# Kernel optimization log

Measured on AMD Instinct MI355X. Metric: run time of the kernel, lower is better.

The kernel has to match this reference:

```python
import jax, jax.numpy as jnp
import numpy as np

B, L, DIM, HEADS = 4, 1024, 512, 8
HD = DIM // HEADS
HID = max(64, DIM // 2)
WIN = 32
SPARSITY = 0.3
TEMP = 1.0
PAT_TAU = 0.5


def setup_inputs() -> dict:
    key = jax.random.key(0)
    ks = jax.random.split(key, 8)
    gn = lambda k, shape, sc: jax.random.normal(k, shape, jnp.float32) * sc
    return {
        "x": jax.random.normal(ks[0], (B, L, DIM), jnp.float32),
        "mask": jnp.ones((B, L), jnp.int32),
        "Wqkv": gn(ks[1], (3 * DIM, DIM), 0.02),
        "Wproj": gn(ks[2], (DIM, DIM), 0.02),
        "bproj": jnp.zeros((DIM,), jnp.float32),
        "Wsel1": gn(ks[3], (HID, DIM), 0.05),
        "bsel1": jnp.zeros((HID,), jnp.float32),
        "Wsel2": gn(ks[4], (3, HID), 0.05),
        "bsel2": jnp.zeros((3,), jnp.float32),
        "log_pattern_tau": jnp.asarray(np.log(PAT_TAU), jnp.float32),
        "sparse_w": gn(ks[5], (HEADS,), 0.2),
        "sparse_b": jnp.zeros((HEADS,), jnp.float32),
    }


def reference(x, mask, Wqkv, Wproj, bproj, Wsel1, bsel1, Wsel2, bsel2,
              log_pattern_tau, sparse_w, sparse_b):
    Bq, Lq, D = x.shape
    scale = HD ** -0.5
    qkv = (x @ Wqkv.T).reshape(Bq, Lq, 3, HEADS, HD)
    q = jnp.transpose(qkv[:, :, 0], (0, 2, 1, 3))  # (B,H,L,hd)
    k = jnp.transpose(qkv[:, :, 1], (0, 2, 1, 3))
    v = jnp.transpose(qkv[:, :, 2], (0, 2, 1, 3))
    scores = jnp.einsum('bhid,bhjd->bhij', q, k) * scale  # (B,H,L,L)

    # pattern selector on mean-pooled features (eval: no gumbel, no dropout)
    pooled = x.mean(axis=1)
    logits = jax.nn.relu(pooled @ Wsel1.T + bsel1) @ Wsel2.T + bsel2  # (B,3)
    tau = jnp.clip(jnp.exp(log_pattern_tau), 1e-4, 10.0)
    pw = jax.nn.softmax(logits / tau, axis=-1)  # (B,3)

    half = WIN // 2
    ii = jnp.arange(Lq)[:, None]
    jj = jnp.arange(Lq)[None, :]
    local = ((jj >= ii - half) & (jj <= ii + half)).astype(jnp.float32)

    # learned sparse top-k mask per head via kth-value threshold
    kk = max(1, int(Lq * (1.0 - SPARSITY)))
    s = scores * sparse_w[None, :, None, None] + sparse_b[None, :, None, None]
    kth = jax.lax.top_k(s, kk)[0][..., -1:]
    smask = (s >= kth).astype(jnp.float32)  # (B,H,L,L)

    combined = (pw[:, 0, None, None, None] * local[None, None]
                + pw[:, 1, None, None, None]
                + pw[:, 2, None, None, None] * smask)
    neg = jnp.float32(-1e9)
    scores = jnp.where(combined > 0.05, scores, neg)
    scores = jnp.where(mask[:, None, None, :] == 0, neg, scores)

    # fallback: if a row is fully masked, unmask position 0
    all_masked = jnp.all(scores <= neg + 1e-6, axis=-1)  # (B,H,L)
    scores = scores.at[..., 0].set(jnp.where(all_masked, 0.0, scores[..., 0]))

    attn = jax.nn.softmax(scores / TEMP, axis=-1)
    out = jnp.einsum('bhij,bhjd->bhid', attn, v)
    out = jnp.transpose(out, (0, 2, 1, 3)).reshape(Bq, Lq, D)
    return out @ Wproj.T + bproj
```

## Files before the change

kernel.cpp:

```cpp
#include <hip/hip_runtime.h>
#include <math.h>

typedef __attribute__((ext_vector_type(8))) short short8;
typedef __attribute__((ext_vector_type(4))) float floatx4;

#define MFMA16(a, b, c) __builtin_amdgcn_mfma_f32_16x16x32_bf16(a, b, c, 0, 0, 0)


#define FRAG512(row, k) (((size_t)((row) >> 4)) * 8192 + (((k) >> 5) * 512) + \
                         ((((k) >> 3) & 3) * 128) + (((row) & 15) * 8) + ((k) & 7))
#define FRAGQK(row, e)  (((size_t)((row) >> 4)) * 1024 + (((e) >> 5) * 512) + \
                         ((((e) >> 3) & 3) * 128) + (((row) & 15) * 8) + ((e) & 7))

#define OFF_XB    ((size_t)0)
#define OFF_WQKV  ((size_t)4194304)
#define OFF_WPROJ ((size_t)5767168)
#define OFF_Q     ((size_t)6291456)
#define OFF_K     ((size_t)10485760)
#define OFF_VT    ((size_t)14680064)
#define OFF_AT    ((size_t)18874368)
#define OFF_PW    ((size_t)23068672)
#define OFF_PAR   ((size_t)23069696)
#define OFF_W1T   ((size_t)23595008)

__device__ __forceinline__ unsigned short f2bf(float f) {
    unsigned u = __float_as_uint(f);
    return (unsigned short)((u + 0x7fffu + ((u >> 16) & 1u)) >> 16);
}
__device__ __forceinline__ float bf2f(unsigned short s) {
    return __uint_as_float((unsigned)s << 16);
}
__device__ __forceinline__ void gl16(const void* g, void* l) {
    __builtin_amdgcn_global_load_lds(
        (const __attribute__((address_space(1))) unsigned*)g,
        (__attribute__((address_space(3))) unsigned*)l, 16, 0, 0);
}

__device__ __forceinline__ void frag_cvt_tile(const float* __restrict__ src,
                                              unsigned short* __restrict__ dst,
                                              const int t, const float sc)
{
    const int ln = t & 15, quad = (t >> 4) & 3, kh = t >> 6;
    #pragma unroll
    for (int i = 0; i < 4; ++i) {
        const int kb = kh + i * 4;
        const float* s = src + (size_t)ln * 512 + kb * 32 + quad * 8;
        float4 f0 = *(const float4*)s;
        float4 f1 = *(const float4*)(s + 4);
        unsigned short o[8] = { f2bf(f0.x * sc), f2bf(f0.y * sc), f2bf(f0.z * sc), f2bf(f0.w * sc),
                                f2bf(f1.x * sc), f2bf(f1.y * sc), f2bf(f1.z * sc), f2bf(f1.w * sc) };
        unsigned short* d = dst + kb * 512 + (size_t)(t & 63) * 8;
        *(ushort4*)d       = make_ushort4(o[0], o[1], o[2], o[3]);
        *(ushort4*)(d + 4) = make_ushort4(o[4], o[5], o[6], o[7]);
    }
}

__global__ __launch_bounds__(256)
void cvt_all(const float* __restrict__ x, const float* __restrict__ wqkv,
             const float* __restrict__ wproj, const float* __restrict__ W1,
             unsigned short* __restrict__ xb, unsigned short* __restrict__ oq,
             unsigned short* __restrict__ op, float* __restrict__ partial,
             float* __restrict__ w1t)
{
    const int bid = blockIdx.x, t = threadIdx.x;
    if (bid < 256) {
        const int rt = bid;
        const float* src = x + (size_t)rt * 16 * 512;
        frag_cvt_tile(src, xb + (size_t)rt * 8192, t, 1.f);
        float s0 = 0.f, s1 = 0.f;
        #pragma unroll 4
        for (int l = 0; l < 16; ++l) {
            s0 += src[(size_t)l * 512 + t];
            s1 += src[(size_t)l * 512 + t + 256];
        }
        partial[(size_t)rt * 512 + t] = s0;
        partial[(size_t)rt * 512 + t + 256] = s1;
    } else if (bid < 384) {
        const int tile = bid - 256;
        if (tile < 96)
            frag_cvt_tile(wqkv + (size_t)tile * 16 * 512, oq + (size_t)tile * 8192, t, 1.f);
        else
            frag_cvt_tile(wproj + (size_t)(tile - 96) * 16 * 512,
                          op + (size_t)(tile - 96) * 8192, t, 1.f);
    } else {
        __shared__ float tl[64][65];
        const int tile = bid - 384;
        const int tr = tile >> 3, tc = tile & 7;
        const int lr = t >> 6, lc = t & 63;
        #pragma unroll
        for (int p = 0; p < 16; ++p) {
            const int r = p * 4 + lr;
            tl[r][lc] = W1[(size_t)(tr * 64 + r) * 512 + tc * 64 + lc];
        }
        __syncthreads();
        #pragma unroll
        for (int p = 0; p < 16; ++p) {
            const int d = p * 4 + lr;
            w1t[(size_t)(tc * 64 + d) * 256 + tr * 64 + lc] = tl[lc][d];
        }
    }
}

__global__ __launch_bounds__(128)
void gemm_qkv_sel(const unsigned short* __restrict__ xb, const unsigned short* __restrict__ wb,
                  unsigned short* __restrict__ qo, unsigned short* __restrict__ ko,
                  unsigned short* __restrict__ vo,
                  const float* __restrict__ partial, const float* __restrict__ w1t,
                  const float* __restrict__ b1, const float* __restrict__ W2,
                  const float* __restrict__ b2, const float* __restrict__ ltau,
                  float* __restrict__ pwout)
{
    __shared__ __align__(16) unsigned short tile[2][64 * 72];
    const int bx = blockIdx.x, by = blockIdx.y;
    const int t = threadIdx.x;
    const int w = t >> 6, l64 = t & 63;

    if (by == 64) {
        if (bx >= 4) return;
        const int b = bx;
        float* pooled = (float*)&tile[0][0];
        float* hpart  = pooled + 512;
        float* h1s    = hpart + 512;
        float* lg     = h1s + 256;
        #pragma unroll
        for (int c = 0; c < 4; ++c) {
            const int col = t + c * 128;
            float s = 0.f;
            for (int p = 0; p < 64; ++p) s += partial[((size_t)b * 64 + p) * 512 + col];
            pooled[col] = s * (1.f / 1024.f);
        }
        __syncthreads();
        {
            float4 acc = make_float4(0.f, 0.f, 0.f, 0.f);
            const float* wt = w1t + (size_t)w * 256 * 256 + l64 * 4;
            for (int d = 0; d < 256; ++d) {
                const float pv = pooled[w * 256 + d];
                float4 wv = *(const float4*)(wt + (size_t)d * 256);
                acc.x += pv * wv.x; acc.y += pv * wv.y;
                acc.z += pv * wv.z; acc.w += pv * wv.w;
            }
            *(float4*)&hpart[w * 256 + l64 * 4] = acc;
        }
        __syncthreads();
        {
            #pragma unroll
            for (int c = 0; c < 2; ++c) {
                const int r = t + c * 128;
                h1s[r] = fmaxf(hpart[r] + hpart[256 + r] + b1[r], 0.f);
            }
        }
        __syncthreads();
        if (t < 3) {
            float s = b2[t];
            const float* w2 = W2 + t * 256;
            for (int i = 0; i < 256; ++i) s += w2[i] * h1s[i];
            float tauv = fminf(fmaxf(expf(ltau[0]), 1e-4f), 10.f);
            lg[t] = s / tauv;
        }
        __syncthreads();
        if (t == 0) {
            float m = fmaxf(lg[0], fmaxf(lg[1], lg[2]));
            float e0 = expf(lg[0] - m), e1 = expf(lg[1] - m), e2 = expf(lg[2] - m);
            float inv = 1.f / (e0 + e1 + e2);
            pwout[b * 3 + 0] = e0 * inv;
            pwout[b * 3 + 1] = e1 * inv;
            pwout[b * 3 + 2] = e2 * inv;
        }
        return;
    }

    const int ln = l64 & 15, quad = l64 >> 4;
    const int m0 = by << 6;
    const int nb0 = (bx << 7) + (w << 6);

    const unsigned short* Abase = xb + ((size_t)(m0 >> 4)) * 8192 + l64 * 8;
    const unsigned short* Bbase = wb + ((size_t)(nb0 >> 4)) * 8192 + l64 * 8;

    floatx4 acc[4][4];
    #pragma unroll
    for (int i = 0; i < 4; ++i)
        #pragma unroll
        for (int j = 0; j < 4; ++j) acc[i][j] = (floatx4){0.f, 0.f, 0.f, 0.f};

    short8 a0[4], b0[4], a1[4], b1v[4];
    #pragma unroll
    for (int i = 0; i < 4; ++i) {
        a0[i] = *(const short8*)(Abase + (size_t)i * 8192);
        b0[i] = *(const short8*)(Bbase + (size_t)i * 8192);
    }
    for (int s = 0; s < 16; s += 2) {
        #pragma unroll
        for (int i = 0; i < 4; ++i) {
            a1[i]  = *(const short8*)(Abase + (size_t)i * 8192 + (s + 1) * 512);
            b1v[i] = *(const short8*)(Bbase + (size_t)i * 8192 + (s + 1) * 512);
        }
        #pragma unroll
        for (int i = 0; i < 4; ++i)
            #pragma unroll
            for (int j = 0; j < 4; ++j)
                acc[i][j] = MFMA16(a0[i], b0[j], acc[i][j]);
        if (s + 2 < 16) {
            #pragma unroll
            for (int i = 0; i < 4; ++i) {
                a0[i] = *(const short8*)(Abase + (size_t)i * 8192 + (s + 2) * 512);
                b0[i] = *(const short8*)(Bbase + (size_t)i * 8192 + (s + 2) * 512);
            }
        }
        #pragma unroll
        for (int i = 0; i < 4; ++i)
            #pragma unroll
            for (int j = 0; j < 4; ++j)
                acc[i][j] = MFMA16(a1[i], b1v[j], acc[i][j]);
    }

    unsigned short* tw = &tile[w][0];
    const int which = bx >> 2;
    const int hh = (nb0 >> 6) & 7;
    const int g = (by >> 4) * 8 + hh;
    const int lrow0 = m0 & 1023;

    if (which == 2) {
        #pragma unroll
        for (int j = 0; j < 4; ++j)
            #pragma unroll
            for (int i = 0; i < 4; ++i)
                #pragma unroll
                for (int reg = 0; reg < 4; ++reg)
                    tw[(j * 16 + ln) * 72 + i * 16 + quad * 4 + reg] = f2bf(acc[i][j][reg]);
        const int chunk = lrow0 >> 7;
        const int ks0 = (lrow0 & 127) >> 5;
        unsigned short* dst = vo + (size_t)g * 65536 + (size_t)chunk * 8192;
        #pragma unroll
        for (int et = 0; et < 4; ++et)
            #pragma unroll
            for (int ksl = 0; ksl < 2; ++ksl) {
                const unsigned short* srcp = &tw[(et * 16 + ln) * 72 + ksl * 32 + quad * 8];
                *(short8*)(dst + (et * 4 + ks0 + ksl) * 512 + l64 * 8) = *(const short8*)srcp;
            }
    } else {
        const float sc = (which == 0) ? 0.125f : 1.f;
        #pragma unroll
        for (int j = 0; j < 4; ++j)
            #pragma unroll
            for (int i = 0; i < 4; ++i)
                #pragma unroll
                for (int reg = 0; reg < 4; ++reg)
                    tw[(i * 16 + quad * 4 + reg) * 72 + j * 16 + ln] = f2bf(acc[i][j][reg] * sc);
        unsigned short* dst = (which == 0 ? qo : ko) + (size_t)g * 65536;
        #pragma unroll
        for (int rt = 0; rt < 4; ++rt)
            #pragma unroll
            for (int eh = 0; eh < 2; ++eh) {
                const unsigned short* srcp = &tw[(rt * 16 + ln) * 72 + eh * 32 + quad * 8];
                *(short8*)(dst + ((size_t)((lrow0 >> 4) + rt)) * 1024 + eh * 512 + l64 * 8) =
                    *(const short8*)srcp;
            }
    }
}

__global__ __launch_bounds__(64)
void gemm_proj(const unsigned short* __restrict__ ab, const unsigned short* __restrict__ wb,
               const float* __restrict__ bias, float* __restrict__ out)
{
    const int t = threadIdx.x;
    const int ln = t & 15, quad = t >> 4;
    const int n0 = blockIdx.x << 6, m0 = blockIdx.y << 5;

    const unsigned short* Abase = ab + ((size_t)(m0 >> 4)) * 8192 + t * 8;
    const unsigned short* Bbase = wb + ((size_t)(n0 >> 4)) * 8192 + t * 8;

    floatx4 acc[2][4];
    #pragma unroll
    for (int i = 0; i < 2; ++i)
        #pragma unroll
        for (int j = 0; j < 4; ++j) acc[i][j] = (floatx4){0.f, 0.f, 0.f, 0.f};

    short8 a0[2], b0[4], a1[2], b1v[4];
    #pragma unroll
    for (int i = 0; i < 2; ++i) a0[i] = *(const short8*)(Abase + (size_t)i * 8192);
    #pragma unroll
    for (int j = 0; j < 4; ++j) b0[j] = *(const short8*)(Bbase + (size_t)j * 8192);
    for (int s = 0; s < 16; s += 2) {
        #pragma unroll
        for (int i = 0; i < 2; ++i) a1[i]  = *(const short8*)(Abase + (size_t)i * 8192 + (s + 1) * 512);
        #pragma unroll
        for (int j = 0; j < 4; ++j) b1v[j] = *(const short8*)(Bbase + (size_t)j * 8192 + (s + 1) * 512);
        #pragma unroll
        for (int i = 0; i < 2; ++i)
            #pragma unroll
            for (int j = 0; j < 4; ++j)
                acc[i][j] = MFMA16(a0[i], b0[j], acc[i][j]);
        if (s + 2 < 16) {
            #pragma unroll
            for (int i = 0; i < 2; ++i) a0[i] = *(const short8*)(Abase + (size_t)i * 8192 + (s + 2) * 512);
            #pragma unroll
            for (int j = 0; j < 4; ++j) b0[j] = *(const short8*)(Bbase + (size_t)j * 8192 + (s + 2) * 512);
        }
        #pragma unroll
        for (int i = 0; i < 2; ++i)
            #pragma unroll
            for (int j = 0; j < 4; ++j)
                acc[i][j] = MFMA16(a1[i], b1v[j], acc[i][j]);
    }
    #pragma unroll
    for (int j = 0; j < 4; ++j) {
        const float bv = bias[n0 + j * 16 + ln];
        #pragma unroll
        for (int i = 0; i < 2; ++i)
            #pragma unroll
            for (int reg = 0; reg < 4; ++reg)
                out[(size_t)(m0 + i * 16 + quad * 4 + reg) * 512 + n0 + j * 16 + ln] =
                    acc[i][j][reg] + bv;
    }
}

__global__ __launch_bounds__(256)
void attn_flash(const unsigned short* __restrict__ qm, const unsigned short* __restrict__ km,
                const unsigned short* __restrict__ vm, const int* __restrict__ mask,
                const float* __restrict__ pw, const float* __restrict__ sw,
                const float* __restrict__ sb, unsigned short* __restrict__ aout)
{
    __shared__ int mk[1024];
    __shared__ __align__(16) unsigned short Ks[8192];
    __shared__ __align__(16) unsigned short Vs[8192];
    __shared__ float PO[4][16][68];
    __shared__ unsigned kths[4][16];

    const int t = threadIdx.x;
    const int w = t >> 6, l64 = t & 63;
    const int ln = l64 & 15, quad = l64 >> 4;
    const int g = blockIdx.x & 31;
    const int rg = blockIdx.x >> 5;
    const int b = g >> 3, h = g & 7;
    const int i0 = rg * 64 + w * 16;

    const unsigned short* qg = qm + (size_t)g * 65536;
    const unsigned short* kg = km + (size_t)g * 65536;
    const unsigned short* vg = vm + (size_t)g * 65536;

    *(int4*)&mk[t * 4] = *(const int4*)(mask + b * 1024 + t * 4);

    const float pw0 = pw[b * 3 + 0], pw1 = pw[b * 3 + 1], pw2 = pw[b * 3 + 2];
    const bool a00 = pw1 > 0.05f;
    const bool a10 = (pw0 * 1.0f + pw1) > 0.05f;
    const bool a01 = (pw1 + pw2) > 0.05f;
    const bool a11 = ((pw0 * 1.0f + pw1) + pw2) > 0.05f;
    const bool need_sparse = (!a00 && a01) || (!a10 && a11);
    const bool flat_ok = (!need_sparse) && a00 && a10;
    const float w_h = sw[h], b_h = sb[h];
    __syncthreads();

    unsigned kth_r[4] = {0u, 0u, 0u, 0u};
    if (need_sparse) {
        unsigned* ub = (unsigned*)&PO[w][0][0];
        for (int r = 0; r < 16; ++r) {
            for (int c = 0; c < 16; ++c) {
                const int col = c * 64 + l64;
                float s = 0.f;
                for (int e = 0; e < 64; ++e)
                    s += bf2f(qg[FRAGQK(i0 + r, e)]) * bf2f(kg[FRAGQK(col, e)]);
                unsigned uu = __float_as_uint(s * w_h + b_h);
                ub[col] = (uu & 0x80000000u) ? ~uu : (uu | 0x80000000u);
            }
            unsigned u[16];
            #pragma unroll
            for (int c = 0; c < 16; ++c) u[c] = ub[l64 + c * 64];
            unsigned act = 0xFFFFu, p = 0u;
            int kk = 716;
            for (int bit = 31; bit >= 0; --bit) {
                unsigned ones = 0u;
                #pragma unroll
                for (int c = 0; c < 16; ++c)
                    if (((act >> c) & 1u) && ((u[c] >> bit) & 1u)) ones |= (1u << c);
                int c1 = __popc(ones);
                for (int off = 32; off; off >>= 1) c1 += __shfl_xor(c1, off);
                if (kk <= c1) { p |= (1u << bit); act &= ones; }
                else          { kk -= c1; act &= ~ones; }
            }
            if (l64 == 0) kths[w][r] = p;
        }
        #pragma unroll
        for (int reg = 0; reg < 4; ++reg) kth_r[reg] = kths[w][quad * 4 + reg];
    }

    const short8 aq0 = *(const short8*)(qg + ((size_t)(i0 >> 4)) * 1024 + l64 * 8);
    const short8 aq1 = *(const short8*)(qg + ((size_t)(i0 >> 4)) * 1024 + 512 + l64 * 8);

    float l_acc[4] = {0.f, 0.f, 0.f, 0.f};
    floatx4 accv[4];
    #pragma unroll
    for (int et = 0; et < 4; ++et) accv[et] = (floatx4){0.f, 0.f, 0.f, 0.f};
    unsigned short* Pw = (unsigned short*)&PO[w][0][0];

    for (int jc = 0; jc < 8; ++jc) {
        const int j0 = jc << 7;
        {
            const unsigned short* kc = kg + (size_t)j0 * 64;
            const unsigned short* vc = vg + ((size_t)(j0 >> 7)) * 8192;
            #pragma unroll
            for (int c = 0; c < 4; ++c) {
                const int bi = w * 4 + c;
                gl16(kc + bi * 512 + l64 * 8, (char*)Ks + bi * 1024);
                gl16(vc + bi * 512 + l64 * 8, (char*)Vs + bi * 1024);
            }
        }
        const bool mall = __all((mk[j0 + l64] != 0) && (mk[j0 + 64 + l64] != 0));
        const bool fast = flat_ok && mall;
        __syncthreads();

        floatx4 sfr[8];
        #pragma unroll
        for (int nt = 0; nt < 8; ++nt) {
            const short8 kb0 = *(const short8*)(Ks + nt * 1024 + l64 * 8);
            const short8 kb1 = *(const short8*)(Ks + nt * 1024 + 512 + l64 * 8);
            floatx4 z = (floatx4){0.f, 0.f, 0.f, 0.f};
            z = MFMA16(aq0, kb0, z);
            z = MFMA16(aq1, kb1, z);
            sfr[nt] = z;
        }

        if (!fast) {
            #pragma unroll
            for (int nt = 0; nt < 8; ++nt) {
                const int j = j0 + nt * 16 + ln;
                const bool mk0 = (mk[j] == 0);
                #pragma unroll
                for (int reg = 0; reg < 4; ++reg) {
                    const int i = i0 + quad * 4 + reg;
                    const float s = sfr[nt][reg];
                    const bool loc = (j >= i - 16) && (j <= i + 16);
                    bool sm = false;
                    if (need_sparse) {
                        unsigned uu = __float_as_uint(s * w_h + b_h);
                        unsigned key = (uu & 0x80000000u) ? ~uu : (uu | 0x80000000u);
                        sm = key >= kth_r[reg];
                    }
                    bool allowed = loc ? (sm ? a11 : a10) : (sm ? a01 : a00);
                    if (mk0) allowed = false;
                    sfr[nt][reg] = allowed ? s : -1e9f;
                }
            }
        }
        #pragma unroll
        for (int nt = 0; nt < 8; ++nt)
            #pragma unroll
            for (int reg = 0; reg < 4; ++reg) {
                const float p = __expf(sfr[nt][reg]);
                l_acc[reg] += p;
                Pw[(quad * 4 + reg) * 136 + nt * 16 + ln] = f2bf(p);
            }
        short8 pa[4];
        #pragma unroll
        for (int ks = 0; ks < 4; ++ks)
            pa[ks] = *(const short8*)&Pw[ln * 136 + ks * 32 + quad * 8];
        #pragma unroll
        for (int et = 0; et < 4; ++et) {
            floatx4 a = accv[et];
            #pragma unroll
            for (int ks = 0; ks < 4; ++ks) {
                const short8 bv = *(const short8*)(Vs + (et * 4 + ks) * 512 + l64 * 8);
                a = MFMA16(pa[ks], bv, a);
            }
            accv[et] = a;
        }
        __syncthreads();
    }

    #pragma unroll
    for (int reg = 0; reg < 4; ++reg) {
        float v = l_acc[reg];
        v += __shfl_xor(v, 1);
        v += __shfl_xor(v, 2);
        v += __shfl_xor(v, 4);
        v += __shfl_xor(v, 8);
        l_acc[reg] = v;
    }

    #pragma unroll
    for (int et = 0; et < 4; ++et)
        #pragma unroll
        for (int reg = 0; reg < 4; ++reg) {
            float val;
            if (l_acc[reg] == 0.f)
                val = bf2f(vg[et * 2048 + ln * 8]);
            else
                val = accv[et][reg] / l_acc[reg];
            PO[w][quad * 4 + reg][et * 16 + ln] = val;
        }
    #pragma unroll
    for (int rr = 0; rr < 4; ++rr) {
        const int r = (l64 >> 4) * 4 + rr;
        const int cb = (l64 & 15) * 4;
        float4 ov = *(const float4*)&PO[w][r][cb];
        ushort4 res = make_ushort4(f2bf(ov.x), f2bf(ov.y), f2bf(ov.z), f2bf(ov.w));
        const int row_g = b * 1024 + i0 + r;
        const int col = h * 64 + cb;
        *(ushort4*)&aout[FRAG512(row_g, col)] = res;
    }
}

extern "C" void kernel_launch(void* const* d_in, const int* in_sizes, int n_in,
                              void* d_out, int out_size, void* d_ws, size_t ws_size,
                              hipStream_t stream) {
    const float* x     = (const float*)d_in[0];
    const int*   mask  = (const int*)d_in[1];
    const float* Wqkv  = (const float*)d_in[2];
    const float* Wproj = (const float*)d_in[3];
    const float* bproj = (const float*)d_in[4];
    const float* Wsel1 = (const float*)d_in[5];
    const float* bsel1 = (const float*)d_in[6];
    const float* Wsel2 = (const float*)d_in[7];
    const float* bsel2 = (const float*)d_in[8];
    const float* ltau  = (const float*)d_in[9];
    const float* sw    = (const float*)d_in[10];
    const float* sb    = (const float*)d_in[11];
    char* ws = (char*)d_ws;
    unsigned short* xb     = (unsigned short*)(ws + OFF_XB);
    unsigned short* wqkvb  = (unsigned short*)(ws + OFF_WQKV);
    unsigned short* wprojb = (unsigned short*)(ws + OFF_WPROJ);
    unsigned short* q      = (unsigned short*)(ws + OFF_Q);
    unsigned short* k      = (unsigned short*)(ws + OFF_K);
    unsigned short* v      = (unsigned short*)(ws + OFF_VT);
    unsigned short* attnb  = (unsigned short*)(ws + OFF_AT);
    float* pw  = (float*)(ws + OFF_PW);
    float* par = (float*)(ws + OFF_PAR);
    float* w1t = (float*)(ws + OFF_W1T);
    float* out = (float*)d_out;
    (void)in_sizes; (void)n_in; (void)out_size; (void)ws_size;

    cvt_all<<<416, 256, 0, stream>>>(x, Wqkv, Wproj, Wsel1, xb, wqkvb, wprojb, par, w1t);
    gemm_qkv_sel<<<dim3(12, 65), 128, 0, stream>>>(xb, wqkvb, q, k, v,
                                                   par, w1t, bsel1, Wsel2, bsel2, ltau, pw);
    attn_flash<<<512, 256, 0, stream>>>(q, k, v, mask, pw, sw, sb, attnb);
    gemm_proj<<<dim3(8, 128), 64, 0, stream>>>(attnb, wprojb, bproj, out);
}
```

Measured before the change: 145.7 us.

## Double-buffer K tiles in attention loop to prefetch next chunk

Each K tile for the next key chunk is now loaded into a second LDS buffer while the current chunk is computed, with the first tile issued before the sparse-threshold prologue. The barrier that used to sit right after the loads moves to just before the P·V MFMAs, so the QK^T MFMAs can run without waiting on the V load. The fp32 output staging and the sparse scratch buffer are aliased into the K buffers to limit LDS growth. Total LDS per block still rises, which may reduce how many blocks fit per CU.

```diff
diff --git a/kernel.cpp b/kernel.cpp
--- a/kernel.cpp
+++ b/kernel.cpp
@@ -321,9 +321,9 @@
                 const float* __restrict__ sb, unsigned short* __restrict__ aout)
 {
     __shared__ int mk[1024];
-    __shared__ __align__(16) unsigned short Ks[8192];
+    __shared__ __align__(16) unsigned short Ks[2][8192];
     __shared__ __align__(16) unsigned short Vs[8192];
-    __shared__ float PO[4][16][68];
+    __shared__ __align__(16) unsigned short Pws[4][2176];
     __shared__ unsigned kths[4][16];
 
     const int t = threadIdx.x;
@@ -348,11 +348,16 @@
     const bool need_sparse = (!a00 && a01) || (!a10 && a11);
     const bool flat_ok = (!need_sparse) && a00 && a10;
     const float w_h = sw[h], b_h = sb[h];
-    __syncthreads();
+
+    #pragma unroll
+    for (int c = 0; c < 4; ++c) {
+        const int bi = w * 4 + c;
+        gl16(kg + bi * 512 + l64 * 8, (char*)Ks[0] + bi * 1024);
+    }
 
     unsigned kth_r[4] = {0u, 0u, 0u, 0u};
     if (need_sparse) {
-        unsigned* ub = (unsigned*)&PO[w][0][0];
+        unsigned* ub = (unsigned*)((char*)Ks + 16384 + w * 4096);
         for (int r = 0; r < 16; ++r) {
             for (int c = 0; c < 16; ++c) {
                 const int col = c * 64 + l64;
@@ -386,33 +391,42 @@
     const short8 aq0 = *(const short8*)(qg + ((size_t)(i0 >> 4)) * 1024 + l64 * 8);
     const short8 aq1 = *(const short8*)(qg + ((size_t)(i0 >> 4)) * 1024 + 512 + l64 * 8);
 
+    __syncthreads();
+
     float l_acc[4] = {0.f, 0.f, 0.f, 0.f};
     floatx4 accv[4];
     #pragma unroll
     for (int et = 0; et < 4; ++et) accv[et] = (floatx4){0.f, 0.f, 0.f, 0.f};
-    unsigned short* Pw = (unsigned short*)&PO[w][0][0];
+    unsigned short* Pw = &Pws[w][0];
 
     for (int jc = 0; jc < 8; ++jc) {
         const int j0 = jc << 7;
+        const int cur = jc & 1;
+        const unsigned short* Kc = &Ks[cur][0];
         {
-            const unsigned short* kc = kg + (size_t)j0 * 64;
-            const unsigned short* vc = vg + ((size_t)(j0 >> 7)) * 8192;
+            const unsigned short* vc = vg + (size_t)jc * 8192;
             #pragma unroll
             for (int c = 0; c < 4; ++c) {
                 const int bi = w * 4 + c;
-                gl16(kc + bi * 512 + l64 * 8, (char*)Ks + bi * 1024);
                 gl16(vc + bi * 512 + l64 * 8, (char*)Vs + bi * 1024);
+            }
+            if (jc < 7) {
+                const unsigned short* kc = kg + (size_t)(jc + 1) * 8192;
+                #pragma unroll
+                for (int c = 0; c < 4; ++c) {
+                    const int bi = w * 4 + c;
+                    gl16(kc + bi * 512 + l64 * 8, (char*)Ks[cur ^ 1] + bi * 1024);
+                }
             }
         }
         const bool mall = __all((mk[j0 + l64] != 0) && (mk[j0 + 64 + l64] != 0));
         const bool fast = flat_ok && mall;
-        __syncthreads();
 
         floatx4 sfr[8];
         #pragma unroll
         for (int nt = 0; nt < 8; ++nt) {
-            const short8 kb0 = *(const short8*)(Ks + nt * 1024 + l64 * 8);
-            const short8 kb1 = *(const short8*)(Ks + nt * 1024 + 512 + l64 * 8);
+            const short8 kb0 = *(const short8*)(Kc + nt * 1024 + l64 * 8);
+            const short8 kb1 = *(const short8*)(Kc + nt * 1024 + 512 + l64 * 8);
             floatx4 z = (floatx4){0.f, 0.f, 0.f, 0.f};
             z = MFMA16(aq0, kb0, z);
             z = MFMA16(aq1, kb1, z);
@@ -453,6 +467,7 @@
         #pragma unroll
         for (int ks = 0; ks < 4; ++ks)
             pa[ks] = *(const short8*)&Pw[ln * 136 + ks * 32 + quad * 8];
+        __syncthreads();
         #pragma unroll
         for (int et = 0; et < 4; ++et) {
             floatx4 a = accv[et];
@@ -476,6 +491,7 @@
         l_acc[reg] = v;
     }
 
+    float* PO_w = (float*)((char*)Ks + w * 4352);
     #pragma unroll
     for (int et = 0; et < 4; ++et)
         #pragma unroll
@@ -485,13 +501,13 @@
                 val = bf2f(vg[et * 2048 + ln * 8]);
             else
                 val = accv[et][reg] / l_acc[reg];
-            PO[w][quad * 4 + reg][et * 16 + ln] = val;
+            PO_w[(quad * 4 + reg) * 68 + et * 16 + ln] = val;
         }
     #pragma unroll
     for (int rr = 0; rr < 4; ++rr) {
         const int r = (l64 >> 4) * 4 + rr;
         const int cb = (l64 & 15) * 4;
-        float4 ov = *(const float4*)&PO[w][r][cb];
+        float4 ov = *(const float4*)&PO_w[r * 68 + cb];
         ushort4 res = make_ushort4(f2bf(ov.x), f2bf(ov.y), f2bf(ov.z), f2bf(ov.w));
         const int row_g = b * 1024 + i0 + r;
         const int col = h * 64 + cb;
```

Measured after the change: 147.1 us. Within noise of the previous version (+1.0%).
